# Kernel tuning notes

Measured on AMD Instinct MI355X. Metric: run time of the kernel, lower is better.

The kernel has to match this reference:

```python
import jax, jax.numpy as jnp
import numpy as np

N, E, ESM, H_DIM, HEADS, LAYERS = 20000, 640000, 1280, 256, 8, 3
C = H_DIM // HEADS  # per-head channels = 32
B, M = 4096, 8


def setup_inputs() -> dict:
    key = jax.random.key(0)
    ks = jax.random.split(key, 24)
    s = lambda i, *shp: jax.random.normal(ks[i], shp, dtype=jnp.float32) * 0.02
    inp = {
        'x': jax.random.normal(ks[0], (N, ESM), dtype=jnp.float32),
        'edge_index': jax.random.randint(ks[1], (2, E), 0, N),
        'sites': jax.random.randint(ks[2], (B, M), 0, N),
        'mut_onehot': jax.random.normal(ks[3], (B, M, 20), dtype=jnp.float32),
        'mask': jnp.ones((B, M), dtype=bool),
        # params
        'in_W': s(4, ESM, H_DIM), 'in_b': jnp.zeros((H_DIM,), jnp.float32),
        'gat_W': s(5, LAYERS, H_DIM, HEADS * C),
        'att_src': s(6, LAYERS, HEADS, C), 'att_dst': s(7, LAYERS, HEADS, C),
        'gat_b': jnp.zeros((LAYERS, H_DIM), jnp.float32),
        'ln_g': jnp.ones((LAYERS, H_DIM), jnp.float32),
        'ln_b': jnp.zeros((LAYERS, H_DIM), jnp.float32),
        'me_W1': s(8, 20, H_DIM), 'me_b1': jnp.zeros((H_DIM,), jnp.float32),
        'me_W2': s(9, H_DIM, H_DIM), 'me_b2': jnp.zeros((H_DIM,), jnp.float32),
        'pool_q': jax.random.normal(ks[10], (H_DIM,), dtype=jnp.float32),
        'key_W': s(11, H_DIM, H_DIM), 'key_b': jnp.zeros((H_DIM,), jnp.float32),
        'mlp_W1': s(12, H_DIM, H_DIM // 2), 'mlp_b1': jnp.zeros((H_DIM // 2,), jnp.float32),
        'mlp_W2': s(13, H_DIM // 2, 1), 'mlp_b2': jnp.zeros((1,), jnp.float32),
    }
    return inp


def layer_norm(h, g, b, eps=1e-5):
    mu = h.mean(-1, keepdims=True)
    var = ((h - mu) ** 2).mean(-1, keepdims=True)
    return (h - mu) * jax.lax.rsqrt(var + eps) * g + b


def gat_conv(h, src, dst, W, a_src, a_dst, b):
    # PyG GATConv: linear -> per-node attn logits -> edge leaky_relu -> segment softmax over dst -> scatter-sum
    xh = (h @ W).reshape(N, HEADS, C)
    al_s = (xh * a_src).sum(-1)  # [N,H]
    al_d = (xh * a_dst).sum(-1)
    alpha = jax.nn.leaky_relu(al_s[src] + al_d[dst], negative_slope=0.2)  # [E',H]
    mx = jax.ops.segment_max(alpha, dst, num_segments=N)
    ea = jnp.exp(alpha - mx[dst])
    denom = jax.ops.segment_sum(ea, dst, num_segments=N)
    w = ea / (denom[dst] + 1e-16)
    msg = xh[src] * w[:, :, None]  # [E',H,C]
    out = jax.ops.segment_sum(msg, dst, num_segments=N)
    return out.reshape(N, HEADS * C) + b


def reference(x, edge_index, sites, mut_onehot, mask, in_W, in_b, gat_W, att_src, att_dst,
              gat_b, ln_g, ln_b, me_W1, me_b1, me_W2, me_b2, pool_q, key_W, key_b,
              mlp_W1, mlp_b1, mlp_W2, mlp_b2):
    # GATConv default add_self_loops=True
    loops = jnp.arange(N, dtype=edge_index.dtype)
    src = jnp.concatenate([edge_index[0], loops])
    dst = jnp.concatenate([edge_index[1], loops])
    # encode_graph (eval mode: dropout = identity)
    h = x @ in_W + in_b
    for i in range(LAYERS):
        h_new = gat_conv(h, src, dst, gat_W[i], att_src[i][None], att_dst[i][None], gat_b[i])
        h_new = jax.nn.elu(h_new)
        h = layer_norm(h_new + h, ln_g[i], ln_b[i])
    # predict_batch
    site_embeds = h[sites]  # [B,M,H_DIM]
    mut_embeds = jax.nn.relu(mut_onehot @ me_W1 + me_b1) @ me_W2 + me_b2
    combined = site_embeds + mut_embeds
    keys = combined @ key_W + key_b
    scores = (pool_q * keys).sum(-1) / np.sqrt(H_DIM).astype(np.float32)
    scores = jnp.where(mask, scores, -jnp.inf)
    weights = jax.nn.softmax(scores, axis=-1)[..., None]
    pooled = (weights * combined).sum(axis=1)  # [B,H_DIM]
    out = jax.nn.relu(pooled @ mlp_W1 + mlp_b1) @ mlp_W2 + mlp_b2
    return out.squeeze(-1)
```

## Files before the change

kernel.cpp:

```cpp
#include <hip/hip_runtime.h>
#include <math.h>

#define N_NODES 20000
#define N_EDGES 640000
#define E_TOT   (N_EDGES + N_NODES)
#define HD 256
#define NH 8
#define CH 32
#define NB 4096
#define NM 8

typedef short bf16x8 __attribute__((ext_vector_type(8)));
typedef float f32x4  __attribute__((ext_vector_type(4)));

__device__ __forceinline__ ushort f2bf(float f) {
  uint u = __float_as_uint(f);
  u += 0x7FFFu + ((u >> 16) & 1u);
  return (ushort)(u >> 16);
}
__device__ __forceinline__ float bf2f(ushort s) {
  return __uint_as_float(((uint)s) << 16);
}

__global__ __launch_bounds__(256) void k_wtrans(
    const float* __restrict__ W, ushort* __restrict__ WT,
    int K, int N, int strideW, int strideWT)
{
  __shared__ float tile[64][65];
  const float* Wp = W + (size_t)blockIdx.z * strideW;
  ushort* WTp = WT + (size_t)blockIdx.z * strideWT;
  int n0 = blockIdx.x * 64, k0 = blockIdx.y * 64;
  int t = threadIdx.x;
  int c = t & 63, r0 = (t >> 6) * 16;
#pragma unroll
  for (int i = 0; i < 16; ++i)
    tile[r0 + i][c] = Wp[(size_t)(k0 + r0 + i) * N + n0 + c];
  __syncthreads();
#pragma unroll
  for (int i = 0; i < 16; ++i)
    WTp[(size_t)(n0 + r0 + i) * K + k0 + c] = f2bf(tile[c][r0 + i]);
}

template<int MODE>
__global__ __launch_bounds__(256, 4) void k_gemm_mfma(
    const void* __restrict__ Ain, const ushort* __restrict__ BT,
    const float* __restrict__ bias, float* __restrict__ Cf,
    ushort* __restrict__ Cb, int M, int K)
{
  __shared__ ushort As[64 * 32];
  __shared__ ushort Bs[128 * 32];
  const int t = threadIdx.x;
  const int n0 = blockIdx.x * 128;
  const int m0 = blockIdx.y * 64;
  const int wave = t >> 6, lane = t & 63;
  const int wm = (wave & 1) * 32, wn = (wave >> 1) * 64;
  const int lm = lane & 15, quad = lane >> 4;

  f32x4 acc[2][4];
#pragma unroll
  for (int mi = 0; mi < 2; ++mi)
#pragma unroll
    for (int ni = 0; ni < 4; ++ni) acc[mi][ni] = (f32x4){0.f, 0.f, 0.f, 0.f};

  const int a_row = t >> 2, a_j = t & 3;
  const int ar = min(m0 + a_row, M - 1);
  const int a_sw = (a_j ^ (a_row & 3)) * 8;

  for (int k0 = 0; k0 < K; k0 += 32) {
    if (MODE == 0) {
      const float* src = (const float*)Ain + (size_t)ar * K + k0 + a_j * 8;
      float4 u = *(const float4*)src;
      float4 v = *(const float4*)(src + 4);
      uint4 p;
      p.x = (uint)f2bf(u.x) | ((uint)f2bf(u.y) << 16);
      p.y = (uint)f2bf(u.z) | ((uint)f2bf(u.w) << 16);
      p.z = (uint)f2bf(v.x) | ((uint)f2bf(v.y) << 16);
      p.w = (uint)f2bf(v.z) | ((uint)f2bf(v.w) << 16);
      *(uint4*)&As[a_row * 32 + a_sw] = p;
    } else {
      const ushort* src = (const ushort*)Ain + (size_t)ar * K + k0 + a_j * 8;
      *(uint4*)&As[a_row * 32 + a_sw] = *(const uint4*)src;
    }
#pragma unroll
    for (int p = 0; p < 2; ++p) {
      int id = t + p * 256;
      int row = id >> 2, j = id & 3;
      *(uint4*)&Bs[row * 32 + ((j ^ (row & 3)) * 8)] =
          *(const uint4*)(BT + (size_t)(n0 + row) * K + k0 + j * 8);
    }
    __syncthreads();
    bf16x8 af[2], bfr[4];
#pragma unroll
    for (int mi = 0; mi < 2; ++mi) {
      int row = wm + mi * 16 + lm;
      af[mi] = *(const bf16x8*)&As[row * 32 + ((quad ^ (row & 3)) << 3)];
    }
#pragma unroll
    for (int ni = 0; ni < 4; ++ni) {
      int row = wn + ni * 16 + lm;
      bfr[ni] = *(const bf16x8*)&Bs[row * 32 + ((quad ^ (row & 3)) << 3)];
    }
#pragma unroll
    for (int mi = 0; mi < 2; ++mi)
#pragma unroll
      for (int ni = 0; ni < 4; ++ni)
        acc[mi][ni] = __builtin_amdgcn_mfma_f32_16x16x32_bf16(af[mi], bfr[ni], acc[mi][ni], 0, 0, 0);
    __syncthreads();
  }

#pragma unroll
  for (int mi = 0; mi < 2; ++mi) {
#pragma unroll
    for (int r = 0; r < 4; ++r) {
      int row = m0 + wm + mi * 16 + quad * 4 + r;
      if (row < M) {
#pragma unroll
        for (int ni = 0; ni < 4; ++ni) {
          int col = n0 + wn + ni * 16 + lm;
          float vv = acc[mi][ni][r];
          if (MODE == 0) {
            float o = vv + bias[col];
            Cf[(size_t)row * HD + col] = o;
            Cb[(size_t)row * HD + col] = f2bf(o);
          } else {
            Cb[(size_t)row * HD + col] = f2bf(vv);
          }
        }
      }
    }
  }
}

__global__ void k_setconst(int* __restrict__ p, int n, int v) {
  int i = blockIdx.x * blockDim.x + threadIdx.x;
  if (i < n) p[i] = v;
}

__global__ void k_count(const int* __restrict__ dst, int* __restrict__ cnt) {
  int e = blockIdx.x * blockDim.x + threadIdx.x;
  if (e < N_EDGES) atomicAdd(&cnt[dst[e]], 1);
}

__global__ __launch_bounds__(1024) void k_scanA(const int* __restrict__ cnt,
                                                int* __restrict__ sc, int* __restrict__ tot) {
  __shared__ int wsum[16];
  int g = blockIdx.x * 1024 + threadIdx.x;
  int lane = threadIdx.x & 63, w = threadIdx.x >> 6;
  int v = (g < N_NODES) ? cnt[g] : 0;
#pragma unroll
  for (int off = 1; off < 64; off <<= 1) {
    int u = __shfl_up(v, off);
    if (lane >= off) v += u;
  }
  if (lane == 63) wsum[w] = v;
  __syncthreads();
  if (w == 0) {
    int s = (lane < 16) ? wsum[lane] : 0;
#pragma unroll
    for (int off = 1; off < 16; off <<= 1) {
      int u = __shfl_up(s, off);
      if (lane >= off) s += u;
    }
    if (lane < 16) wsum[lane] = s;
  }
  __syncthreads();
  if (w > 0) v += wsum[w - 1];
  if (g < N_NODES) sc[g] = v;
  if (threadIdx.x == 1023) tot[blockIdx.x] = v;
}

__global__ void k_scanB(int* __restrict__ tot) {
  int lane = threadIdx.x;
  int v = (lane < 20) ? tot[lane] : 0;
#pragma unroll
  for (int off = 1; off < 32; off <<= 1) {
    int u = __shfl_up(v, off);
    if (lane >= off) v += u;
  }
  int e = __shfl_up(v, 1);
  if (lane == 0) e = 0;
  if (lane < 20) tot[lane] = e;
}

__global__ __launch_bounds__(1024) void k_scanC(const int* __restrict__ sc,
                                                const int* __restrict__ tot,
                                                int* __restrict__ row_ptr) {
  int g = blockIdx.x * 1024 + threadIdx.x;
  if (g < N_NODES) row_ptr[g + 1] = sc[g] + tot[blockIdx.x];
  if (g == 0) row_ptr[0] = 0;
}

__global__ void k_fill(const int* __restrict__ ei, const int* __restrict__ row_ptr,
                       int* __restrict__ fill, int* __restrict__ csr) {
  int idx = blockIdx.x * blockDim.x + threadIdx.x;
  if (idx >= E_TOT) return;
  int s, d;
  if (idx < N_EDGES) { s = ei[idx]; d = ei[N_EDGES + idx]; }
  else               { s = idx - N_EDGES; d = s; }
  int p = atomicAdd(&fill[d], 1);
  csr[row_ptr[d] + p] = s;
}

__global__ void k_attn(const ushort* __restrict__ xh,
                       const float* __restrict__ att_s,
                       const float* __restrict__ att_d,
                       float* __restrict__ al_s, float* __restrict__ al_d)
{
  int idx = blockIdx.x * blockDim.x + threadIdx.x;
  if (idx >= N_NODES * NH) return;
  int hh = idx & 7;
  const ushort* row = xh + (size_t)(idx >> 3) * HD + hh * CH;
  const float4* a4  = (const float4*)(att_s + hh * CH);
  const float4* b4  = (const float4*)(att_d + hh * CH);
  float s = 0.f, d = 0.f;
#pragma unroll
  for (int q = 0; q < 8; ++q) {
    ushort4 xv = *(const ushort4*)(row + q * 4);
    float4 a = a4[q], b = b4[q];
    float v0 = bf2f(xv.x), v1 = bf2f(xv.y), v2 = bf2f(xv.z), v3 = bf2f(xv.w);
    s += v0 * a.x + v1 * a.y + v2 * a.z + v3 * a.w;
    d += v0 * b.x + v1 * b.y + v2 * b.z + v3 * b.w;
  }
  al_s[idx] = s;
  al_d[idx] = d;
}

__global__ __launch_bounds__(256) void k_aggregate(
    const ushort* __restrict__ xh, const float* __restrict__ al_s,
    const float* __restrict__ al_d, const int* __restrict__ row_ptr,
    const int* __restrict__ csr_src, const float* __restrict__ gat_b,
    const float* __restrict__ ln_g, const float* __restrict__ ln_b,
    float* __restrict__ h, ushort* __restrict__ h_bf)
{
  __shared__ float s_ea[4][64][9];
  __shared__ int   s_src[4][64];
  __shared__ int   s_deg[4];
  const int t = threadIdx.x;
  const int w = t >> 6, lane = t & 63;
  const int lane32 = lane & 31, hw = lane >> 5;
  const int node = blockIdx.x * 4 + w;
  const int base = row_ptr[node];
  const int deg  = row_ptr[node + 1] - base;
  if (lane == 0) s_deg[w] = deg;
  __syncthreads();
  const int maxdeg = max(max(s_deg[0], s_deg[1]), max(s_deg[2], s_deg[3]));
  const int chunks = (maxdeg + 63) >> 6;

  float ald[8];
  {
    float4 a0 = *(const float4*)(al_d + (size_t)node * NH);
    float4 a1 = *(const float4*)(al_d + (size_t)node * NH + 4);
    ald[0] = a0.x; ald[1] = a0.y; ald[2] = a0.z; ald[3] = a0.w;
    ald[4] = a1.x; ald[5] = a1.y; ald[6] = a1.z; ald[7] = a1.w;
  }
  const int myhead = lane32 >> 2;
  float acc[8] = {0.f, 0.f, 0.f, 0.f, 0.f, 0.f, 0.f, 0.f};
  float den = 0.f;

  for (int c = 0; c < chunks; ++c) {
    const int cs = c << 6;
    int n = deg - cs; n = (n > 64) ? 64 : n;
    if (lane < n) {
      int s = csr_src[base + cs + lane];
      s_src[w][lane] = s;
      float4 b0 = *(const float4*)(al_s + (size_t)s * NH);
      float4 b1 = *(const float4*)(al_s + (size_t)s * NH + 4);
      float al[8] = {b0.x, b0.y, b0.z, b0.w, b1.x, b1.y, b1.z, b1.w};
#pragma unroll
      for (int q = 0; q < 8; ++q) {
        float a = al[q] + ald[q];
        a = fmaxf(a, 0.2f * a);
        s_ea[w][lane][q] = __expf(a);
      }
    }
    __syncthreads();
    for (int e = 0; e < n; e += 2) {
      int my_e = e + hw;
      if (my_e < n) {
        int s = s_src[w][my_e];
        float wa = s_ea[w][my_e][myhead];
        den += wa;
        uint4 xv = *(const uint4*)(xh + (size_t)s * HD + lane32 * 8);
        ushort e0 = (ushort)(xv.x & 0xFFFF), e1 = (ushort)(xv.x >> 16);
        ushort e2 = (ushort)(xv.y & 0xFFFF), e3 = (ushort)(xv.y >> 16);
        ushort e4 = (ushort)(xv.z & 0xFFFF), e5 = (ushort)(xv.z >> 16);
        ushort e6 = (ushort)(xv.w & 0xFFFF), e7 = (ushort)(xv.w >> 16);
        acc[0] = fmaf(wa, bf2f(e0), acc[0]);
        acc[1] = fmaf(wa, bf2f(e1), acc[1]);
        acc[2] = fmaf(wa, bf2f(e2), acc[2]);
        acc[3] = fmaf(wa, bf2f(e3), acc[3]);
        acc[4] = fmaf(wa, bf2f(e4), acc[4]);
        acc[5] = fmaf(wa, bf2f(e5), acc[5]);
        acc[6] = fmaf(wa, bf2f(e6), acc[6]);
        acc[7] = fmaf(wa, bf2f(e7), acc[7]);
      }
    }
    __syncthreads();
  }

#pragma unroll
  for (int q = 0; q < 8; ++q) acc[q] += __shfl_xor(acc[q], 32);
  den += __shfl_xor(den, 32);

  const float inv = 1.f / (den + 1e-16f);
  const int c8 = lane32 * 8;
  float4 g0 = *(const float4*)(gat_b + c8);
  float4 g1 = *(const float4*)(gat_b + c8 + 4);
  float gb[8] = {g0.x, g0.y, g0.z, g0.w, g1.x, g1.y, g1.z, g1.w};
  float4 h0 = *(const float4*)(h + (size_t)node * HD + c8);
  float4 h1 = *(const float4*)(h + (size_t)node * HD + c8 + 4);
  float hr[8] = {h0.x, h0.y, h0.z, h0.w, h1.x, h1.y, h1.z, h1.w};
  float v[8], sum8 = 0.f;
#pragma unroll
  for (int q = 0; q < 8; ++q) {
    float vv = acc[q] * inv + gb[q];
    vv = (vv > 0.f) ? vv : (__expf(vv) - 1.f);
    vv += hr[q];
    v[q] = vv;
    sum8 += vv;
  }
#pragma unroll
  for (int off = 32; off > 0; off >>= 1) sum8 += __shfl_xor(sum8, off);
  const float mu = sum8 * (1.f / 512.f);
  float ss8 = 0.f;
#pragma unroll
  for (int q = 0; q < 8; ++q) {
    v[q] -= mu;
    ss8 = fmaf(v[q], v[q], ss8);
  }
#pragma unroll
  for (int off = 32; off > 0; off >>= 1) ss8 += __shfl_xor(ss8, off);
  const float r = rsqrtf(ss8 * (1.f / 512.f) + 1e-5f);
  if (hw == 0) {
    float4 lg0 = *(const float4*)(ln_g + c8);
    float4 lg1 = *(const float4*)(ln_g + c8 + 4);
    float4 lb0 = *(const float4*)(ln_b + c8);
    float4 lb1 = *(const float4*)(ln_b + c8 + 4);
    float lg[8] = {lg0.x, lg0.y, lg0.z, lg0.w, lg1.x, lg1.y, lg1.z, lg1.w};
    float lb[8] = {lb0.x, lb0.y, lb0.z, lb0.w, lb1.x, lb1.y, lb1.z, lb1.w};
    float o[8];
#pragma unroll
    for (int q = 0; q < 8; ++q) o[q] = v[q] * r * lg[q] + lb[q];
    float4 of0 = {o[0], o[1], o[2], o[3]};
    float4 of1 = {o[4], o[5], o[6], o[7]};
    *(float4*)(h + (size_t)node * HD + c8) = of0;
    *(float4*)(h + (size_t)node * HD + c8 + 4) = of1;
    uint4 ob;
    ob.x = (uint)f2bf(o[0]) | ((uint)f2bf(o[1]) << 16);
    ob.y = (uint)f2bf(o[2]) | ((uint)f2bf(o[3]) << 16);
    ob.z = (uint)f2bf(o[4]) | ((uint)f2bf(o[5]) << 16);
    ob.w = (uint)f2bf(o[6]) | ((uint)f2bf(o[7]) << 16);
    *(uint4*)(h_bf + (size_t)node * HD + c8) = ob;
  }
}

__global__ __launch_bounds__(256) void k_qk(const float* __restrict__ key_W,
                                            const float* __restrict__ key_b,
                                            const float* __restrict__ pool_q,
                                            float* __restrict__ qk)
{
  __shared__ float sq[HD];
  int t = threadIdx.x;
  sq[t] = pool_q[t];
  __syncthreads();
  float a = 0.f;
  for (int j = 0; j < HD; ++j) a = fmaf(key_W[(size_t)t * HD + j], sq[j], a);
  qk[t] = a;
  if (t == 0) {
    float qb = 0.f;
    for (int j = 0; j < HD; ++j) qb += sq[j] * key_b[j];
    qk[HD] = qb;
  }
}

__global__ __launch_bounds__(256) void k_mut1(
    const float* __restrict__ onehot, const float* __restrict__ W1,
    const float* __restrict__ b1, ushort* __restrict__ m1)
{
  __shared__ float s_oh[128][20];
  const int t = threadIdx.x;
  const int r0 = blockIdx.x * 128;
  float wreg[20];
#pragma unroll
  for (int j = 0; j < 20; ++j) wreg[j] = W1[j * HD + t];
  const float bb = b1[t];
  for (int i = t; i < 128 * 20; i += 256)
    s_oh[i / 20][i % 20] = onehot[(size_t)r0 * 20 + i];
  __syncthreads();
  for (int r = 0; r < 128; ++r) {
    float v = bb;
#pragma unroll
    for (int j = 0; j < 20; ++j) v = fmaf(s_oh[r][j], wreg[j], v);
    m1[(size_t)(r0 + r) * HD + t] = f2bf(fmaxf(v, 0.f));
  }
}

__global__ __launch_bounds__(256, 2) void k_gemm_mut2(
    const ushort* __restrict__ m1, const ushort* __restrict__ W2T,
    const float* __restrict__ me_b2, const float* __restrict__ h,
    const int* __restrict__ sites, const unsigned char* __restrict__ mask8,
    const float* __restrict__ qk, float* __restrict__ pooled)
{
  __shared__ ushort As[64 * 32];
  __shared__ ushort Bs[256 * 32];
  __shared__ float s_part[64][4];
  __shared__ float s_w[64];
  __shared__ int   s_site[64];
  const int t = threadIdx.x;
  const int rows0 = blockIdx.x * 64;
  const int wave = t >> 6, lane = t & 63;
  const int wn = wave * 64;
  const int lm = lane & 15, quad = lane >> 4;

  if (t < 64) s_site[t] = sites[rows0 + t];

  f32x4 acc[4][4];
#pragma unroll
  for (int mi = 0; mi < 4; ++mi)
#pragma unroll
    for (int ni = 0; ni < 4; ++ni) acc[mi][ni] = (f32x4){0.f, 0.f, 0.f, 0.f};

  const int a_row = t >> 2, a_j = t & 3;
  for (int k0 = 0; k0 < HD; k0 += 32) {
    *(uint4*)&As[a_row * 32 + ((a_j ^ (a_row & 3)) * 8)] =
        *(const uint4*)(m1 + (size_t)(rows0 + a_row) * HD + k0 + a_j * 8);
#pragma unroll
    for (int p = 0; p < 4; ++p) {
      int id = t + p * 256;
      int row = id >> 2, j = id & 3;
      *(uint4*)&Bs[row * 32 + ((j ^ (row & 3)) * 8)] =
          *(const uint4*)(W2T + (size_t)row * HD + k0 + j * 8);
    }
    __syncthreads();
    bf16x8 af[4], bfr[4];
#pragma unroll
    for (int mi = 0; mi < 4; ++mi) {
      int row = mi * 16 + lm;
      af[mi] = *(const bf16x8*)&As[row * 32 + ((quad ^ (row & 3)) << 3)];
    }
#pragma unroll
    for (int ni = 0; ni < 4; ++ni) {
      int row = wn + ni * 16 + lm;
      bfr[ni] = *(const bf16x8*)&Bs[row * 32 + ((quad ^ (row & 3)) << 3)];
    }
#pragma unroll
    for (int mi = 0; mi < 4; ++mi)
#pragma unroll
      for (int ni = 0; ni < 4; ++ni)
        acc[mi][ni] = __builtin_amdgcn_mfma_f32_16x16x32_bf16(af[mi], bfr[ni], acc[mi][ni], 0, 0, 0);
    __syncthreads();
  }

  float pscore[4][4];
#pragma unroll
  for (int mi = 0; mi < 4; ++mi)
#pragma unroll
    for (int r = 0; r < 4; ++r) pscore[mi][r] = 0.f;

#pragma unroll
  for (int ni = 0; ni < 4; ++ni) {
    int col = wn + ni * 16 + lm;
    float qkc = qk[col];
    float b2c = me_b2[col];
#pragma unroll
    for (int mi = 0; mi < 4; ++mi) {
#pragma unroll
      for (int r = 0; r < 4; ++r) {
        int row = mi * 16 + quad * 4 + r;
        float c = acc[mi][ni][r] + b2c + h[(size_t)s_site[row] * HD + col];
        acc[mi][ni][r] = c;
        pscore[mi][r] = fmaf(c, qkc, pscore[mi][r]);
      }
    }
  }
#pragma unroll
  for (int mi = 0; mi < 4; ++mi)
#pragma unroll
    for (int r = 0; r < 4; ++r) {
      float p = pscore[mi][r];
      p += __shfl_xor(p, 8); p += __shfl_xor(p, 4);
      p += __shfl_xor(p, 2); p += __shfl_xor(p, 1);
      pscore[mi][r] = p;
    }
  if (lm == 0) {
#pragma unroll
    for (int mi = 0; mi < 4; ++mi)
#pragma unroll
      for (int r = 0; r < 4; ++r)
        s_part[mi * 16 + quad * 4 + r][wave] = pscore[mi][r];
  }
  __syncthreads();
  if (t < 64) {
    float s = s_part[t][0] + s_part[t][1] + s_part[t][2] + s_part[t][3];
    s = (s + qk[HD]) * 0.0625f;
    int grow = rows0 + t;
    bool mb;
    if (mask8[1] != 0) mb = mask8[grow] != 0;
    else               mb = ((const int*)mask8)[grow] != 0;
    s_w[t] = mb ? s : -INFINITY;
  }
  __syncthreads();
  if (t < 8) {
    float e[NM], mx = -INFINITY, den = 0.f;
#pragma unroll
    for (int m = 0; m < NM; ++m) mx = fmaxf(mx, s_w[t * NM + m]);
#pragma unroll
    for (int m = 0; m < NM; ++m) { e[m] = __expf(s_w[t * NM + m] - mx); den += e[m]; }
    float inv = 1.f / den;
#pragma unroll
    for (int m = 0; m < NM; ++m) s_w[t * NM + m] = e[m] * inv;
  }
  __syncthreads();
#pragma unroll
  for (int ni = 0; ni < 4; ++ni) {
    int col = wn + ni * 16 + lm;
#pragma unroll
    for (int mi = 0; mi < 4; ++mi) {
      float pp = 0.f;
#pragma unroll
      for (int r = 0; r < 4; ++r)
        pp = fmaf(s_w[mi * 16 + quad * 4 + r], acc[mi][ni][r], pp);
      pp += __shfl_xor(pp, 16);
      int b = mi * 2 + (quad >> 1);
      if ((quad & 1) == 0)
        pooled[(size_t)(blockIdx.x * 8 + b) * HD + col] = pp;
    }
  }
}

__global__ __launch_bounds__(128) void k_mlp(
    const float* __restrict__ pooled, const float* __restrict__ W1,
    const float* __restrict__ b1, const float* __restrict__ W2,
    const float* __restrict__ b2, float* __restrict__ out)
{
  __shared__ float s_p[16][256];
  __shared__ float s_red[16][128];
  const int t = threadIdx.x;
  const int r0 = blockIdx.x * 16;
  for (int i = t; i < 16 * 256; i += 128) {
    int r = i >> 8, cc = i & 255;
    s_p[r][cc] = pooled[(size_t)(r0 + r) * HD + cc];
  }
  __syncthreads();
  float accm[16];
#pragma unroll
  for (int r = 0; r < 16; ++r) accm[r] = 0.f;
  for (int i = 0; i < 256; ++i) {
    float w = W1[(size_t)i * 128 + t];
#pragma unroll
    for (int r = 0; r < 16; ++r) accm[r] = fmaf(s_p[r][i], w, accm[r]);
  }
  float w2 = W2[t], bb1 = b1[t];
#pragma unroll
  for (int r = 0; r < 16; ++r) s_red[r][t] = fmaxf(accm[r] + bb1, 0.f) * w2;
  __syncthreads();
  if (t < 16) {
    float s = b2[0];
    for (int j = 0; j < 128; ++j) s += s_red[t][j];
    out[r0 + t] = s;
  }
}

extern "C" void kernel_launch(void* const* d_in, const int* in_sizes, int n_in,
                              void* d_out, int out_size, void* d_ws, size_t ws_size,
                              hipStream_t stream) {
  (void)in_sizes; (void)n_in; (void)out_size; (void)ws_size;
  const float* x        = (const float*)d_in[0];
  const int*   ei       = (const int*)d_in[1];
  const int*   sites    = (const int*)d_in[2];
  const float* onehot   = (const float*)d_in[3];
  const unsigned char* mask = (const unsigned char*)d_in[4];
  const float* in_W     = (const float*)d_in[5];
  const float* in_b     = (const float*)d_in[6];
  const float* gat_W    = (const float*)d_in[7];
  const float* att_src  = (const float*)d_in[8];
  const float* att_dst  = (const float*)d_in[9];
  const float* gat_b    = (const float*)d_in[10];
  const float* ln_g     = (const float*)d_in[11];
  const float* ln_b     = (const float*)d_in[12];
  const float* me_W1    = (const float*)d_in[13];
  const float* me_b1    = (const float*)d_in[14];
  const float* me_W2    = (const float*)d_in[15];
  const float* me_b2    = (const float*)d_in[16];
  const float* pool_q   = (const float*)d_in[17];
  const float* key_W    = (const float*)d_in[18];
  const float* key_b    = (const float*)d_in[19];
  const float* mlp_W1   = (const float*)d_in[20];
  const float* mlp_b1   = (const float*)d_in[21];
  const float* mlp_W2   = (const float*)d_in[22];
  const float* mlp_b2   = (const float*)d_in[23];
  float* outp = (float*)d_out;

  char* w = (char*)d_ws;
  float*  h       = (float*)(w + 0);
  ushort* h_bf    = (ushort*)(w + 20480000);
  ushort* xh_bf   = (ushort*)(w + 30720000);
  float*  al_s    = (float*)(w + 40960000);
  float*  al_d    = (float*)(w + 41600000);
  int*    row_ptr = (int*)  (w + 42240000);
  int*    cnt     = (int*)  (w + 42320128);
  int*    csr     = (int*)  (w + 42400128);
  float*  qk      = (float*)(w + 45040128);
  float*  pooled  = (float*)(w + 45041408);
  int*    sc      = (int*)pooled;
  int*    tot     = sc + N_NODES;
  ushort* in_WT   = (ushort*)((char*)pooled + 131072);
  ushort* gat_WT  = (ushort*)((char*)pooled + 786432);
  ushort* m1      = (ushort*)(w + 20480000);
  ushort* me_W2T  = (ushort*)(w + 40960000);

  k_wtrans<<<dim3(4, 20, 1), 256, 0, stream>>>(in_W, in_WT, 1280, HD, 0, 0);
  k_wtrans<<<dim3(4, 4, 3), 256, 0, stream>>>(gat_W, gat_WT, HD, HD, HD * HD, HD * HD);

  k_gemm_mfma<0><<<dim3(2, 313), 256, 0, stream>>>(x, in_WT, in_b, h, h_bf, N_NODES, 1280);

  k_setconst<<<(N_NODES + 255) / 256, 256, 0, stream>>>(cnt, N_NODES, 1);
  k_count<<<(N_EDGES + 255) / 256, 256, 0, stream>>>(ei + N_EDGES, cnt);
  k_scanA<<<20, 1024, 0, stream>>>(cnt, sc, tot);
  k_scanB<<<1, 64, 0, stream>>>(tot);
  k_scanC<<<20, 1024, 0, stream>>>(sc, tot, row_ptr);
  k_setconst<<<(N_NODES + 255) / 256, 256, 0, stream>>>(cnt, N_NODES, 0);
  k_fill<<<(E_TOT + 255) / 256, 256, 0, stream>>>(ei, row_ptr, cnt, csr);

  for (int l = 0; l < 3; ++l) {
    k_gemm_mfma<1><<<dim3(2, 313), 256, 0, stream>>>(h_bf, gat_WT + (size_t)l * HD * HD,
                                                     nullptr, nullptr, xh_bf, N_NODES, HD);
    k_attn<<<(N_NODES * NH + 255) / 256, 256, 0, stream>>>(xh_bf, att_src + l * NH * CH,
                                                           att_dst + l * NH * CH, al_s, al_d);
    k_aggregate<<<N_NODES / 4, 256, 0, stream>>>(xh_bf, al_s, al_d, row_ptr, csr,
                                                 gat_b + l * HD, ln_g + l * HD, ln_b + l * HD,
                                                 h, h_bf);
  }

  k_wtrans<<<dim3(4, 4, 1), 256, 0, stream>>>(me_W2, me_W2T, HD, HD, 0, 0);
  k_mut1<<<NB * NM / 128, 256, 0, stream>>>(onehot, me_W1, me_b1, m1);
  k_qk<<<1, 256, 0, stream>>>(key_W, key_b, pool_q, qk);
  k_gemm_mut2<<<NB * NM / 64, 256, 0, stream>>>(m1, me_W2T, me_b2, h, sites, mask, qk, pooled);
  k_mlp<<<NB / 16, 128, 0, stream>>>(pooled, mlp_W1, mlp_b1, mlp_W2, mlp_b2, outp);
}
```

Measured before the change: 621.7 us.

## Double-buffer GEMM tiles with direct global-to-LDS loads and register prefetch

Turns the MFMA GEMM main loop into a double-buffered pipeline. The next K-tile of B (and A in bf16 mode) is fetched with global_load_lds straight into the alternate LDS buffer, and the fp32 A path prefetches two tiles ahead into registers. The aim is to overlap global-memory latency with MFMA work and to cut VGPR round trips and one barrier per iteration. LDS use doubles, which may lower occupancy. Correctness depends on the swizzle matching the per-lane layout of global_load_lds.

```diff
diff --git a/kernel.cpp b/kernel.cpp
--- a/kernel.cpp
+++ b/kernel.cpp
@@ -22,6 +22,12 @@
   return __uint_as_float(((uint)s) << 16);
 }
 
+__device__ __forceinline__ void gl_lds16(const ushort* g, ushort* l) {
+  __builtin_amdgcn_global_load_lds(
+      (const __attribute__((address_space(1))) void*)g,
+      (__attribute__((address_space(3))) void*)l, 16, 0, 0);
+}
+
 __global__ __launch_bounds__(256) void k_wtrans(
     const float* __restrict__ W, ushort* __restrict__ WT,
     int K, int N, int strideW, int strideWT)
@@ -47,8 +53,8 @@
     const float* __restrict__ bias, float* __restrict__ Cf,
     ushort* __restrict__ Cb, int M, int K)
 {
-  __shared__ ushort As[64 * 32];
-  __shared__ ushort Bs[128 * 32];
+  __shared__ ushort As[2][64 * 32];
+  __shared__ ushort Bs[2][128 * 32];
   const int t = threadIdx.x;
   const int n0 = blockIdx.x * 128;
   const int m0 = blockIdx.y * 64;
@@ -56,49 +62,71 @@
   const int wm = (wave & 1) * 32, wn = (wave >> 1) * 64;
   const int lm = lane & 15, quad = lane >> 4;
 
-  f32x4 acc[2][4];
-#pragma unroll
-  for (int mi = 0; mi < 2; ++mi)
-#pragma unroll
-    for (int ni = 0; ni < 4; ++ni) acc[mi][ni] = (f32x4){0.f, 0.f, 0.f, 0.f};
-
+  const int rl   = lane >> 2;
+  const int jsw  = (lane & 3) ^ (rl & 3);
+  const ushort* Bbase = BT + (size_t)(n0 + 32 * wave) * K;
+  int a1_row = m0 + 16 * wave + rl;
+  a1_row = min(a1_row, M - 1);
   const int a_row = t >> 2, a_j = t & 3;
   const int ar = min(m0 + a_row, M - 1);
   const int a_sw = (a_j ^ (a_row & 3)) * 8;
 
-  for (int k0 = 0; k0 < K; k0 += 32) {
-    if (MODE == 0) {
-      const float* src = (const float*)Ain + (size_t)ar * K + k0 + a_j * 8;
-      float4 u = *(const float4*)src;
-      float4 v = *(const float4*)(src + 4);
-      uint4 p;
-      p.x = (uint)f2bf(u.x) | ((uint)f2bf(u.y) << 16);
-      p.y = (uint)f2bf(u.z) | ((uint)f2bf(u.w) << 16);
-      p.z = (uint)f2bf(v.x) | ((uint)f2bf(v.y) << 16);
-      p.w = (uint)f2bf(v.z) | ((uint)f2bf(v.w) << 16);
-      *(uint4*)&As[a_row * 32 + a_sw] = p;
-    } else {
-      const ushort* src = (const ushort*)Ain + (size_t)ar * K + k0 + a_j * 8;
-      *(uint4*)&As[a_row * 32 + a_sw] = *(const uint4*)src;
-    }
-#pragma unroll
-    for (int p = 0; p < 2; ++p) {
-      int id = t + p * 256;
-      int row = id >> 2, j = id & 3;
-      *(uint4*)&Bs[row * 32 + ((j ^ (row & 3)) * 8)] =
-          *(const uint4*)(BT + (size_t)(n0 + row) * K + k0 + j * 8);
-    }
-    __syncthreads();
+  f32x4 acc[2][4];
+#pragma unroll
+  for (int mi = 0; mi < 2; ++mi)
+#pragma unroll
+    for (int ni = 0; ni < 4; ++ni) acc[mi][ni] = (f32x4){0.f, 0.f, 0.f, 0.f};
+
+  const int T = K >> 5;
+  float4 au, av;
+
+#define ISSUE_B(buf, K0)                                                       \
+  { _Pragma("unroll")                                                          \
+    for (int p = 0; p < 2; ++p)                                                \
+      gl_lds16(Bbase + (size_t)(16 * p + rl) * K + (K0) + jsw * 8,             \
+               &Bs[buf][(32 * wave + 16 * p) * 32]); }
+#define ISSUE_A1(buf, K0)                                                      \
+  gl_lds16((const ushort*)Ain + (size_t)a1_row * K + (K0) + jsw * 8,           \
+           &As[buf][16 * wave * 32]);
+#define LOAD_A0(K0)                                                            \
+  { const float* src = (const float*)Ain + (size_t)ar * K + (K0) + a_j * 8;    \
+    au = *(const float4*)src; av = *(const float4*)(src + 4); }
+#define STORE_A0(buf)                                                          \
+  { uint4 p;                                                                   \
+    p.x = (uint)f2bf(au.x) | ((uint)f2bf(au.y) << 16);                         \
+    p.y = (uint)f2bf(au.z) | ((uint)f2bf(au.w) << 16);                         \
+    p.z = (uint)f2bf(av.x) | ((uint)f2bf(av.y) << 16);                         \
+    p.w = (uint)f2bf(av.z) | ((uint)f2bf(av.w) << 16);                         \
+    *(uint4*)&As[buf][a_row * 32 + a_sw] = p; }
+
+  if (MODE == 0) {
+    LOAD_A0(0);
+    STORE_A0(0);
+    if (T > 1) LOAD_A0(32);
+  } else {
+    ISSUE_A1(0, 0);
+  }
+  ISSUE_B(0, 0);
+  __syncthreads();
+
+  for (int i = 0; i < T; ++i) {
+    const int cur = i & 1;
+    if (i + 1 < T) {
+      if (MODE == 0) STORE_A0(cur ^ 1)
+      else           ISSUE_A1(cur ^ 1, (i + 1) * 32);
+      ISSUE_B(cur ^ 1, (i + 1) * 32);
+      if (MODE == 0 && i + 2 < T) LOAD_A0((i + 2) * 32);
+    }
     bf16x8 af[2], bfr[4];
 #pragma unroll
     for (int mi = 0; mi < 2; ++mi) {
       int row = wm + mi * 16 + lm;
-      af[mi] = *(const bf16x8*)&As[row * 32 + ((quad ^ (row & 3)) << 3)];
+      af[mi] = *(const bf16x8*)&As[cur][row * 32 + ((quad ^ (row & 3)) << 3)];
     }
 #pragma unroll
     for (int ni = 0; ni < 4; ++ni) {
       int row = wn + ni * 16 + lm;
-      bfr[ni] = *(const bf16x8*)&Bs[row * 32 + ((quad ^ (row & 3)) << 3)];
+      bfr[ni] = *(const bf16x8*)&Bs[cur][row * 32 + ((quad ^ (row & 3)) << 3)];
     }
 #pragma unroll
     for (int mi = 0; mi < 2; ++mi)
@@ -107,6 +135,10 @@
         acc[mi][ni] = __builtin_amdgcn_mfma_f32_16x16x32_bf16(af[mi], bfr[ni], acc[mi][ni], 0, 0, 0);
     __syncthreads();
   }
+#undef ISSUE_B
+#undef ISSUE_A1
+#undef LOAD_A0
+#undef STORE_A0
 
 #pragma unroll
   for (int mi = 0; mi < 2; ++mi) {
```

After: 622.9 us. Within noise of the previous version (+0.2%).

## Double-buffer GEMM B tile and load A fragments directly into registers

Applied to the files above, without the earlier changes.

Restructures the MFMA GEMM main loop so the B tile is double-buffered in shared memory and the next k-slice's global loads are issued before the current slice's MFMAs. The A operand no longer goes through LDS: each lane loads its fragment straight from global memory into registers, converting from fp32 in MODE 0. The aim is to overlap global latency with compute and cut one LDS round trip plus a barrier per step. The cost is more registers and uncoalesced per-lane A reads, and the loop assumes K/32 is even.

```diff
diff --git a/kernel.cpp b/kernel.cpp
--- a/kernel.cpp
+++ b/kernel.cpp
@@ -21,6 +21,14 @@
 __device__ __forceinline__ float bf2f(ushort s) {
   return __uint_as_float(((uint)s) << 16);
 }
+__device__ __forceinline__ bf16x8 cvt8(float4 u, float4 v) {
+  bf16x8 r;
+  r[0] = (short)f2bf(u.x); r[1] = (short)f2bf(u.y);
+  r[2] = (short)f2bf(u.z); r[3] = (short)f2bf(u.w);
+  r[4] = (short)f2bf(v.x); r[5] = (short)f2bf(v.y);
+  r[6] = (short)f2bf(v.z); r[7] = (short)f2bf(v.w);
+  return r;
+}
 
 __global__ __launch_bounds__(256) void k_wtrans(
     const float* __restrict__ W, ushort* __restrict__ WT,
@@ -47,8 +55,7 @@
     const float* __restrict__ bias, float* __restrict__ Cf,
     ushort* __restrict__ Cb, int M, int K)
 {
-  __shared__ ushort As[64 * 32];
-  __shared__ ushort Bs[128 * 32];
+  __shared__ ushort Bs[2][128 * 32];
   const int t = threadIdx.x;
   const int n0 = blockIdx.x * 128;
   const int m0 = blockIdx.y * 64;
@@ -56,57 +63,83 @@
   const int wm = (wave & 1) * 32, wn = (wave >> 1) * 64;
   const int lm = lane & 15, quad = lane >> 4;
 
+  int arow[2];
+#pragma unroll
+  for (int mi = 0; mi < 2; ++mi)
+    arow[mi] = min(m0 + wm + mi * 16 + lm, M - 1);
+
+  const int b_row0 = t >> 2, b_j0 = t & 3;
+  const int b_row1 = (t + 256) >> 2, b_j1 = (t + 256) & 3;
+
   f32x4 acc[2][4];
 #pragma unroll
   for (int mi = 0; mi < 2; ++mi)
 #pragma unroll
     for (int ni = 0; ni < 4; ++ni) acc[mi][ni] = (f32x4){0.f, 0.f, 0.f, 0.f};
 
-  const int a_row = t >> 2, a_j = t & 3;
-  const int ar = min(m0 + a_row, M - 1);
-  const int a_sw = (a_j ^ (a_row & 3)) * 8;
-
-  for (int k0 = 0; k0 < K; k0 += 32) {
-    if (MODE == 0) {
-      const float* src = (const float*)Ain + (size_t)ar * K + k0 + a_j * 8;
-      float4 u = *(const float4*)src;
-      float4 v = *(const float4*)(src + 4);
-      uint4 p;
-      p.x = (uint)f2bf(u.x) | ((uint)f2bf(u.y) << 16);
-      p.y = (uint)f2bf(u.z) | ((uint)f2bf(u.w) << 16);
-      p.z = (uint)f2bf(v.x) | ((uint)f2bf(v.y) << 16);
-      p.w = (uint)f2bf(v.z) | ((uint)f2bf(v.w) << 16);
-      *(uint4*)&As[a_row * 32 + a_sw] = p;
-    } else {
-      const ushort* src = (const ushort*)Ain + (size_t)ar * K + k0 + a_j * 8;
-      *(uint4*)&As[a_row * 32 + a_sw] = *(const uint4*)src;
-    }
-#pragma unroll
-    for (int p = 0; p < 2; ++p) {
-      int id = t + p * 256;
-      int row = id >> 2, j = id & 3;
-      *(uint4*)&Bs[row * 32 + ((j ^ (row & 3)) * 8)] =
-          *(const uint4*)(BT + (size_t)(n0 + row) * K + k0 + j * 8);
-    }
+  float4 fa[2][2][2];
+  bf16x8 af[2][2];
+  uint4  br[2];
+
+#define LOAD_A(S, K0)                                                          \
+  { _Pragma("unroll")                                                          \
+    for (int mi = 0; mi < 2; ++mi) {                                           \
+      if (MODE == 0) {                                                         \
+        const float* p = (const float*)Ain + (size_t)arow[mi] * K + (K0) + quad * 8; \
+        fa[S][mi][0] = *(const float4*)p;                                      \
+        fa[S][mi][1] = *(const float4*)(p + 4);                                \
+      } else {                                                                 \
+        af[S][mi] = *(const bf16x8*)((const ushort*)Ain + (size_t)arow[mi] * K + (K0) + quad * 8); \
+      }                                                                        \
+    } }
+#define CVT_A(S)                                                               \
+  { if (MODE == 0) {                                                           \
+      _Pragma("unroll")                                                        \
+      for (int mi = 0; mi < 2; ++mi)                                           \
+        af[S][mi] = cvt8(fa[S][mi][0], fa[S][mi][1]);                          \
+    } }
+#define LOAD_B(K0)                                                             \
+  { br[0] = *(const uint4*)(BT + (size_t)(n0 + b_row0) * K + (K0) + b_j0 * 8); \
+    br[1] = *(const uint4*)(BT + (size_t)(n0 + b_row1) * K + (K0) + b_j1 * 8); }
+#define STORE_B(BUF)                                                           \
+  { *(uint4*)&Bs[BUF][b_row0 * 32 + ((b_j0 ^ (b_row0 & 3)) * 8)] = br[0];      \
+    *(uint4*)&Bs[BUF][b_row1 * 32 + ((b_j1 ^ (b_row1 & 3)) * 8)] = br[1]; }
+#define COMPUTE(BUF, S)                                                        \
+  { CVT_A(S)                                                                   \
+    _Pragma("unroll")                                                          \
+    for (int ni = 0; ni < 4; ++ni) {                                           \
+      int row = wn + ni * 16 + lm;                                             \
+      bf16x8 bfr = *(const bf16x8*)&Bs[BUF][row * 32 + ((quad ^ (row & 3)) << 3)]; \
+      _Pragma("unroll")                                                        \
+      for (int mi = 0; mi < 2; ++mi)                                           \
+        acc[mi][ni] = __builtin_amdgcn_mfma_f32_16x16x32_bf16(af[S][mi], bfr, acc[mi][ni], 0, 0, 0); \
+    } }
+
+  const int T = K >> 5;
+  LOAD_A(0, 0);
+  LOAD_B(0);
+  STORE_B(0);
+  __syncthreads();
+
+  for (int i = 0; i < T; i += 2) {
+    LOAD_A(1, (i + 1) * 32);
+    LOAD_B((i + 1) * 32);
+    COMPUTE(0, 0);
+    STORE_B(1);
     __syncthreads();
-    bf16x8 af[2], bfr[4];
-#pragma unroll
-    for (int mi = 0; mi < 2; ++mi) {
-      int row = wm + mi * 16 + lm;
-      af[mi] = *(const bf16x8*)&As[row * 32 + ((quad ^ (row & 3)) << 3)];
-    }
-#pragma unroll
-    for (int ni = 0; ni < 4; ++ni) {
-      int row = wn + ni * 16 + lm;
-      bfr[ni] = *(const bf16x8*)&Bs[row * 32 + ((quad ^ (row & 3)) << 3)];
-    }
-#pragma unroll
-    for (int mi = 0; mi < 2; ++mi)
-#pragma unroll
-      for (int ni = 0; ni < 4; ++ni)
-        acc[mi][ni] = __builtin_amdgcn_mfma_f32_16x16x32_bf16(af[mi], bfr[ni], acc[mi][ni], 0, 0, 0);
+    if (i + 2 < T) {
+      LOAD_A(0, (i + 2) * 32);
+      LOAD_B((i + 2) * 32);
+    }
+    COMPUTE(1, 1);
+    if (i + 2 < T) STORE_B(0);
     __syncthreads();
   }
+#undef LOAD_A
+#undef CVT_A
+#undef LOAD_B
+#undef STORE_B
+#undef COMPUTE
 
 #pragma unroll
   for (int mi = 0; mi < 2; ++mi) {
```

Measured after the change: 697.3 us. +12.2%, slower.
